# Optimization experiments

Hardware: AMD Instinct MI355X
Metric: run time of the kernel (lower is better)

Reference implementation:

```python
import jax, jax.numpy as jnp
import numpy as np

EPS = 1e-5
DILATIONS = (1, 2, 4)


def conv2d(x, w, b, pad, groups=1, dil=1):
    # x [B,C,H,W], w [O, C//groups, kh, kw]
    y = jax.lax.conv_general_dilated(
        x, w, window_strides=(1, 1),
        padding=[(pad[0], pad[0]), (pad[1], pad[1])],
        rhs_dilation=(dil, dil),
        dimension_numbers=('NCHW', 'OIHW', 'NCHW'),
        feature_group_count=groups)
    return y + b[None, :, None, None]


def bn(x, p):
    # inference BatchNorm2d; p rows = gamma, beta, mean, var
    g, b, m, v = p[0], p[1], p[2], p[3]
    scale = g * jax.lax.rsqrt(v + EPS)
    return x * scale[None, :, None, None] + (b - m * scale)[None, :, None, None]


def bilinear_sample(img, yy, xx):
    # img [C,H,W]; yy,xx [K,H,W] float sampling coords; zero outside -> [C,K,H,W]
    H, W = img.shape[1], img.shape[2]
    y0f = jnp.floor(yy); x0f = jnp.floor(xx)
    wy1 = yy - y0f; wy0 = 1.0 - wy1
    wx1 = xx - x0f; wx0 = 1.0 - wx1

    def gather(yi, xi):
        valid = (yi >= 0) & (yi < H) & (xi >= 0) & (xi < W)
        yc = jnp.clip(yi, 0, H - 1).astype(jnp.int32)
        xc = jnp.clip(xi, 0, W - 1).astype(jnp.int32)
        v = img[:, yc, xc]  # [C,K,H,W]
        return v * valid.astype(img.dtype)

    y1f = y0f + 1.0; x1f = x0f + 1.0
    return (gather(y0f, x0f) * (wy0 * wx0) + gather(y0f, x1f) * (wy0 * wx1)
            + gather(y1f, x0f) * (wy1 * wx0) + gather(y1f, x1f) * (wy1 * wx1))


def deform_depthwise(x, off, weight, dil):
    # torchvision DeformConv2d, groups=C, kernel 3x3, stride 1, pad=dil, no bias.
    # x [B,C,H,W], off [B,18,H,W] (per-kernel-point (dy,dx)), weight [C,3,3]
    B, C, H, W = x.shape
    off = off.reshape(B, 9, 2, H, W)
    hh = jnp.arange(H, dtype=x.dtype)[:, None]
    ww = jnp.arange(W, dtype=x.dtype)[None, :]
    k = jnp.arange(3, dtype=x.dtype) - 1.0
    ky = jnp.repeat(k, 3)  # [9] row offsets
    kx = jnp.tile(k, 3)    # [9] col offsets
    w9 = weight.reshape(C, 9)

    def per_batch(xb, offb):
        yy = offb[:, 0] + hh[None] + (ky * dil)[:, None, None]  # [9,H,W]
        xx = offb[:, 1] + ww[None] + (kx * dil)[:, None, None]
        s = bilinear_sample(xb, yy, xx)  # [C,9,H,W]
        return jnp.einsum('ckhw,ck->chw', s, w9)

    return jax.vmap(per_batch)(x, off)


def setup_inputs() -> dict:
    key = jax.random.key(0)
    ks = jax.random.split(key, 20)
    B, C, H, W = 2, 64, 192, 192
    r = jax.random.normal
    u = lambda k, s: jax.random.uniform(k, s, minval=0.5, maxval=1.5)
    return {
        'x': r(ks[0], (B, C, H, W)),
        'w_off1': r(ks[1], (C, 1, 1, 15)) * 0.1, 'b_off1': r(ks[2], (C,)) * 0.1,
        'bn_off1': u(ks[3], (4, C)),
        'w_off2': r(ks[4], (C, 1, 15, 1)) * 0.1, 'b_off2': r(ks[5], (C,)) * 0.1,
        'bn_off2': u(ks[6], (4, C)),
        'w_off3': r(ks[7], (C, 1, 3, 3)) * 0.1, 'b_off3': r(ks[8], (C,)) * 0.1,
        'bn_off3': u(ks[9], (4, C)),
        'w_bal_off': r(ks[10], (18, C, 1, 1)) * 0.1, 'b_bal_off': r(ks[11], (18,)) * 0.1,
        'bn_bal_off': u(ks[12], (4, 18)),
        'w_def': r(ks[13], (3, C, 3, 3)) * 0.1,
        'w_bal': r(ks[14], (C, C, 1, 1)) * 0.1, 'b_bal': r(ks[15], (C,)) * 0.1,
        'bn_bal': u(ks[16], (4, C)),
    }


def reference(x, w_off1, b_off1, bn_off1, w_off2, b_off2, bn_off2,
              w_off3, b_off3, bn_off3, w_bal_off, b_bal_off, bn_bal_off,
              w_def, w_bal, b_bal, bn_bal):
    C = x.shape[1]
    # DirectionOffsets: three depthwise conv+BN branches summed, then 1x1 conv+BN -> 18ch
    off_sum = (bn(conv2d(x, w_off1, b_off1, (0, 7), groups=C), bn_off1)
               + bn(conv2d(x, w_off2, b_off2, (7, 0), groups=C), bn_off2)
               + bn(conv2d(x, w_off3, b_off3, (1, 1), groups=C), bn_off3))
    offsets = bn(conv2d(off_sum, w_bal_off, b_bal_off, (0, 0)), bn_bal_off)  # [B,18,H,W]
    # sum of depthwise deformable conv branches (shared offsets, different dilation)
    deform_sum = sum(deform_depthwise(x, offsets, w_def[i], float(d))
                     for i, d in enumerate(DILATIONS))
    # final balance (1x1 conv + BN) gated by x
    return bn(conv2d(deform_sum, w_bal, b_bal, (0, 0)), bn_bal) * x
```

## Files before the change

### kernel.cpp

```cpp
#include <hip/hip_runtime.h>
#include <stdint.h>

constexpr int B = 2, C = 64, H = 192, W = 192;
constexpr int HW = H * W;
constexpr int P = B * H * W;
constexpr float EPS = 1e-5f;

__device__ __forceinline__ int swz(int bid, int nwg) {
  return (bid & 7) * (nwg >> 3) + (bid >> 3);
}

__global__ __launch_bounds__(256) void k_prepw(const float* __restrict__ w1,
    const float* __restrict__ w2, const float* __restrict__ w3,
    const float* __restrict__ wdef, float* __restrict__ w1t,
    float* __restrict__ w2t, float* __restrict__ w3t, float* __restrict__ wdeft) {
  int gid = blockIdx.x * 256 + threadIdx.x;
  const int stride = 8 * 256;
  for (int i = gid; i < 960; i += stride) {
    int c = i & 63, j = i >> 6;
    w1t[i] = w1[c * 15 + j];
    w2t[i] = w2[c * 15 + j];
  }
  for (int i = gid; i < 576; i += stride) {
    int c = i & 63, j = i >> 6;
    w3t[i] = w3[c * 9 + j];
  }
  for (int i = gid; i < 1728; i += stride) {
    int c = i & 63, jk = i >> 6;
    int di = jk / 9, k = jk % 9;
    wdeft[i] = wdef[di * (C * 9) + c * 9 + k];
  }
}

__global__ __launch_bounds__(256) void k_transpose(const float* __restrict__ x,
                                                   float* __restrict__ xt) {
  int blk = swz(blockIdx.x, B * H * (W / 64));
  int wt  = blk % (W / 64);
  int h   = (blk / (W / 64)) % H;
  int b   = blk / ((W / 64) * H);
  int w0  = wt * 64;
  __shared__ float tile[64][65];
  int tx = threadIdx.x & 63;
  int ty = threadIdx.x >> 6;
  #pragma unroll
  for (int c = ty; c < 64; c += 4)
    tile[c][tx] = x[((b * C + c) * H + h) * W + w0 + tx];
  __syncthreads();
  #pragma unroll
  for (int wi = ty; wi < 64; wi += 4)
    xt[((b * H + h) * W + w0 + wi) * 64 + tx] = tile[tx][wi];
}

__global__ __launch_bounds__(256) void k_offpipe(const float* __restrict__ xt,
    const float* __restrict__ w1t, const float* __restrict__ b1, const float* __restrict__ bn1,
    const float* __restrict__ w2t, const float* __restrict__ b2, const float* __restrict__ bn2,
    const float* __restrict__ w3t, const float* __restrict__ b3, const float* __restrict__ bn3,
    const float* __restrict__ wq, const float* __restrict__ bq, const float* __restrict__ bnq,
    float* __restrict__ offs) {
  __shared__ float os[16][68];
  __shared__ float wqs[18][66];
  __shared__ float qsc[18], qsh[18];

  int blk = swz(blockIdx.x, P / 16);
  int w0t = (blk % (W / 16)) * 16;
  int h   = (blk / (W / 16)) % H;
  int b   = blk / ((W / 16) * H);
  int wl  = threadIdx.x >> 6;
  int c   = threadIdx.x & 63;
  int w0  = w0t + wl * 4;
  const float* xb = xt + (size_t)b * HW * 64 + c;

  for (int i = threadIdx.x; i < 18 * 64; i += 256)
    wqs[i >> 6][i & 63] = wq[i];
  if (threadIdx.x < 18) {
    int o = threadIdx.x;
    float sc = bnq[o] / sqrtf(bnq[54 + o] + EPS);
    qsc[o] = sc;
    qsh[o] = fmaf(bq[o], sc, bnq[18 + o] - bnq[36 + o] * sc);
  }

  float s1[4] = {0.f, 0.f, 0.f, 0.f};
  float s2[4] = {0.f, 0.f, 0.f, 0.f};
  float s3[4] = {0.f, 0.f, 0.f, 0.f};
  {
    float xv[18];
    #pragma unroll
    for (int j = 0; j < 18; ++j) {
      int ww = w0 - 7 + j;
      xv[j] = (ww >= 0 && ww < W) ? xb[(h * W + ww) * 64] : 0.f;
    }
    #pragma unroll
    for (int j = 0; j < 15; ++j) {
      float wj = w1t[j * 64 + c];
      #pragma unroll
      for (int p = 0; p < 4; ++p) s1[p] = fmaf(xv[p + j], wj, s1[p]);
    }
  }
  #pragma unroll
  for (int j = 0; j < 15; ++j) {
    int hh = h - 7 + j;
    if (hh >= 0 && hh < H) {
      float wj = w2t[j * 64 + c];
      #pragma unroll
      for (int p = 0; p < 4; ++p)
        s2[p] = fmaf(xb[(hh * W + w0 + p) * 64], wj, s2[p]);
    }
  }
  #pragma unroll
  for (int dy = -1; dy <= 1; ++dy) {
    int hh = h + dy;
    if (hh >= 0 && hh < H) {
      float rv[6];
      #pragma unroll
      for (int j = 0; j < 6; ++j) {
        int ww = w0 - 1 + j;
        rv[j] = (ww >= 0 && ww < W) ? xb[(hh * W + ww) * 64] : 0.f;
      }
      #pragma unroll
      for (int dx = 0; dx < 3; ++dx) {
        float wj = w3t[((dy + 1) * 3 + dx) * 64 + c];
        #pragma unroll
        for (int p = 0; p < 4; ++p) s3[p] = fmaf(rv[p + dx], wj, s3[p]);
      }
    }
  }
  float sc1 = bn1[c] / sqrtf(bn1[192 + c] + EPS);
  float sh1 = bn1[64 + c] - bn1[128 + c] * sc1;
  float sc2 = bn2[c] / sqrtf(bn2[192 + c] + EPS);
  float sh2 = bn2[64 + c] - bn2[128 + c] * sc2;
  float sc3 = bn3[c] / sqrtf(bn3[192 + c] + EPS);
  float sh3 = bn3[64 + c] - bn3[128 + c] * sc3;
  float bb1 = b1[c], bb2 = b2[c], bb3 = b3[c];
  #pragma unroll
  for (int p = 0; p < 4; ++p)
    os[wl * 4 + p][c] =
        fmaf(s1[p] + bb1, sc1, sh1) + fmaf(s2[p] + bb2, sc2, sh2) +
        fmaf(s3[p] + bb3, sc3, sh3);
  __syncthreads();

  int p  = threadIdx.x & 15;
  int og = threadIdx.x >> 4;
  float dreg[64];
  #pragma unroll
  for (int q = 0; q < 16; ++q) {
    float4 v = *(float4*)&os[p][q * 4];
    dreg[4 * q + 0] = v.x; dreg[4 * q + 1] = v.y;
    dreg[4 * q + 2] = v.z; dreg[4 * q + 3] = v.w;
  }
  size_t pix = (size_t)((b * H + h) * W + w0t + p);
  #pragma unroll
  for (int pass = 0; pass < 2; ++pass) {
    int o = (pass == 0) ? og : 16 + og;
    if (pass == 1 && og >= 2) break;
    float a0 = 0.f, a1 = 0.f, a2 = 0.f, a3 = 0.f;
    #pragma unroll
    for (int q = 0; q < 16; ++q) {
      float4 ww = *(float4*)&wqs[o][q * 4];
      a0 = fmaf(dreg[4 * q + 0], ww.x, a0);
      a1 = fmaf(dreg[4 * q + 1], ww.y, a1);
      a2 = fmaf(dreg[4 * q + 2], ww.z, a2);
      a3 = fmaf(dreg[4 * q + 3], ww.w, a3);
    }
    float s = (a0 + a1) + (a2 + a3);
    offs[pix * 18 + o] = fmaf(s, qsc[o], qsh[o]);
  }
}

__global__ __launch_bounds__(256) void k_deform(const float* __restrict__ xt,
                                                const float* __restrict__ offs,
                                                const float* __restrict__ wdeft,
                                                float* __restrict__ dsum) {
  __shared__ uint32_t lpre[4][27 * 8 + 4];
  int wl   = threadIdx.x >> 6;
  int lane = threadIdx.x & 63;
  int pix  = swz(blockIdx.x, P / 4) * 4 + wl;

  if (lane < 27) {
    int di = lane / 9, k = lane % 9;
    int d  = 1 << di;
    int w = pix % W, h = (pix / W) % H;
    float offy = offs[(size_t)pix * 18 + 2 * k];
    float offx = offs[(size_t)pix * 18 + 2 * k + 1];
    int ky = k / 3 - 1, kx = k % 3 - 1;
    float yy = (offy + (float)h) + (float)(ky * d);
    float xx = (offx + (float)w) + (float)(kx * d);
    float y0f = floorf(yy), x0f = floorf(xx);
    float wy1 = yy - y0f, wx1 = xx - x0f;
    float wy0 = 1.f - wy1, wx0 = 1.f - wx1;
    int y0 = (int)fmaxf(fminf(y0f, 1.0e4f), -1.0e4f);
    int x0 = (int)fmaxf(fminf(x0f, 1.0e4f), -1.0e4f);
    int y1 = y0 + 1, x1 = x0 + 1;
    float my0 = (y0 >= 0 && y0 < H) ? 1.f : 0.f;
    float my1 = (y1 >= 0 && y1 < H) ? 1.f : 0.f;
    float mx0 = (x0 >= 0 && x0 < W) ? 1.f : 0.f;
    float mx1 = (x1 >= 0 && x1 < W) ? 1.f : 0.f;
    int y0c = min(max(y0, 0), H - 1), y1c = min(max(y1, 0), H - 1);
    int x0c = min(max(x0, 0), W - 1), x1c = min(max(x1, 0), W - 1);
    int r0 = y0c * W, r1 = y1c * W;
    float wy0m = wy0 * my0, wy1m = wy1 * my1;
    float wx0m = wx0 * mx0, wx1m = wx1 * mx1;
    uint32_t* q = &lpre[wl][lane * 8];
    q[0] = (uint32_t)(r0 + x0c) << 8;
    q[1] = (uint32_t)(r0 + x1c) << 8;
    q[2] = (uint32_t)(r1 + x0c) << 8;
    q[3] = (uint32_t)(r1 + x1c) << 8;
    q[4] = __float_as_uint(wy0m * wx0m);
    q[5] = __float_as_uint(wy0m * wx1m);
    q[6] = __float_as_uint(wy1m * wx0m);
    q[7] = __float_as_uint(wy1m * wx1m);
  }
  __syncthreads();

  int c = lane;
  int b = pix / HW;
  const char* xb0 = (const char*)(xt + (size_t)b * HW * 64);

  float wd[27];
  #pragma unroll
  for (int i = 0; i < 27; ++i) wd[i] = wdeft[i * 64 + c];

  float acc = 0.f;
  #pragma unroll
  for (int t = 0; t < 27; ++t) {
    uint4 ov = *(const uint4*)&lpre[wl][t * 8];
    uint4 wv = *(const uint4*)&lpre[wl][t * 8 + 4];
    int s00 = __builtin_amdgcn_readfirstlane((int)ov.x);
    int s01 = __builtin_amdgcn_readfirstlane((int)ov.y);
    int s10 = __builtin_amdgcn_readfirstlane((int)ov.z);
    int s11 = __builtin_amdgcn_readfirstlane((int)ov.w);
    const float* p00 = (const float*)(xb0 + s00);
    const float* p01 = (const float*)(xb0 + s01);
    const float* p10 = (const float*)(xb0 + s10);
    const float* p11 = (const float*)(xb0 + s11);
    float v00 = p00[c], v01 = p01[c], v10 = p10[c], v11 = p11[c];
    float bil = fmaf(v11, __uint_as_float(wv.w),
                 fmaf(v10, __uint_as_float(wv.z),
                  fmaf(v01, __uint_as_float(wv.y),
                       v00 * __uint_as_float(wv.x))));
    acc = fmaf(wd[t], bil, acc);
  }
  dsum[(size_t)pix * 64 + c] = acc;
}

__global__ __launch_bounds__(256) void k_final(const float* __restrict__ ds,
    const float* __restrict__ x, const float* __restrict__ wb,
    const float* __restrict__ bb, const float* __restrict__ bnb,
    float* __restrict__ out) {
  int blk = swz(blockIdx.x, P / 64);
  int w0 = (blk % (W / 64)) * 64;
  int h  = (blk / (W / 64)) % H;
  int b  = blk / ((W / 64) * H);
  __shared__ float dtile[64][68];
  __shared__ float scs[64], shb[64];
  int tx = threadIdx.x & 63;
  int ty = threadIdx.x >> 6;
  int pixbase = (b * H + h) * W + w0;

  {
    int pr  = threadIdx.x >> 4;
    int ic4 = (threadIdx.x & 15) * 4;
    #pragma unroll
    for (int pass = 0; pass < 4; ++pass) {
      int pix = pass * 16 + pr;
      float4 v = *(const float4*)&ds[(size_t)(pixbase + pix) * 64 + ic4];
      *(float4*)&dtile[pix][ic4] = v;
    }
  }
  if (threadIdx.x < 64) {
    float g = bnb[threadIdx.x], vv = bnb[192 + threadIdx.x];
    float sc = g / sqrtf(vv + EPS);
    scs[threadIdx.x] = sc;
    shb[threadIdx.x] = fmaf(bb[threadIdx.x], sc,
                            bnb[64 + threadIdx.x] - bnb[128 + threadIdx.x] * sc);
  }
  __syncthreads();

  float dreg[64];
  #pragma unroll
  for (int q = 0; q < 16; ++q) {
    float4 v = *(float4*)&dtile[tx][q * 4];
    dreg[4 * q + 0] = v.x; dreg[4 * q + 1] = v.y;
    dreg[4 * q + 2] = v.z; dreg[4 * q + 3] = v.w;
  }

  int ocb = __builtin_amdgcn_readfirstlane(ty);
  #pragma unroll
  for (int j = 0; j < 16; ++j) {
    int oc = ocb + 4 * j;
    const float* wr = wb + oc * 64;
    float a0 = 0.f, a1 = 0.f, a2 = 0.f, a3 = 0.f;
    #pragma unroll
    for (int q = 0; q < 16; ++q) {
      a0 = fmaf(dreg[4 * q + 0], wr[4 * q + 0], a0);
      a1 = fmaf(dreg[4 * q + 1], wr[4 * q + 1], a1);
      a2 = fmaf(dreg[4 * q + 2], wr[4 * q + 2], a2);
      a3 = fmaf(dreg[4 * q + 3], wr[4 * q + 3], a3);
    }
    float s = (a0 + a1) + (a2 + a3);
    float val = fmaf(s, scs[oc], shb[oc]);
    int xi = ((b * C + oc) * H + h) * W + w0 + tx;
    out[xi] = val * x[xi];
  }
}

extern "C" void kernel_launch(void* const* d_in, const int* in_sizes, int n_in,
                              void* d_out, int out_size, void* d_ws, size_t ws_size,
                              hipStream_t stream) {
  const float* x     = (const float*)d_in[0];
  const float* w1    = (const float*)d_in[1];
  const float* b1    = (const float*)d_in[2];
  const float* bn1   = (const float*)d_in[3];
  const float* w2    = (const float*)d_in[4];
  const float* b2    = (const float*)d_in[5];
  const float* bn2   = (const float*)d_in[6];
  const float* w3    = (const float*)d_in[7];
  const float* b3    = (const float*)d_in[8];
  const float* bn3   = (const float*)d_in[9];
  const float* wbo   = (const float*)d_in[10];
  const float* bbo   = (const float*)d_in[11];
  const float* bnbo  = (const float*)d_in[12];
  const float* wdef  = (const float*)d_in[13];
  const float* wbal  = (const float*)d_in[14];
  const float* bbal  = (const float*)d_in[15];
  const float* bnbal = (const float*)d_in[16];
  float* out = (float*)d_out;

  float* xt    = (float*)d_ws;
  float* dsum  = xt + (size_t)P * 64;
  float* offs  = dsum + (size_t)P * 64;
  float* wts   = offs + (size_t)P * 18;
  float* w1t   = wts;
  float* w2t   = wts + 960;
  float* w3t   = wts + 1920;
  float* wdeft = wts + 2496;

  k_prepw<<<8, 256, 0, stream>>>(w1, w2, w3, wdef, w1t, w2t, w3t, wdeft);
  k_transpose<<<B * H * (W / 64), 256, 0, stream>>>(x, xt);
  k_offpipe<<<P / 16, 256, 0, stream>>>(xt, w1t, b1, bn1, w2t, b2, bn2,
                                        w3t, b3, bn3, wbo, bbo, bnbo, offs);
  k_deform<<<P / 4, 256, 0, stream>>>(xt, offs, wdeft, dsum);
  k_final<<<P / 64, 256, 0, stream>>>(dsum, x, wbal, bbal, bnbal, out);
}
```

Before: 244.7 us.

## Keep deform sample coords in registers, dedupe center taps, fold weight prep

The per-pixel bilinear sample coordinates and weights are now computed in registers by every lane and broadcast with readlane, replacing the LDS staging buffer and the block barrier. The center tap (k=4) is the same for all three dilations, so it is sampled once and reused for the three weights, dropping two of the 27 gathers per pixel. The separate weight-transpose kernel is merged into the transpose kernel to save one launch. All lanes now repeat the coordinate math, which adds some redundant ALU work.

```diff
diff --git a/kernel.cpp b/kernel.cpp
--- a/kernel.cpp
+++ b/kernel.cpp
@@ -10,30 +10,30 @@
   return (bid & 7) * (nwg >> 3) + (bid >> 3);
 }
 
-__global__ __launch_bounds__(256) void k_prepw(const float* __restrict__ w1,
-    const float* __restrict__ w2, const float* __restrict__ w3,
-    const float* __restrict__ wdef, float* __restrict__ w1t,
-    float* __restrict__ w2t, float* __restrict__ w3t, float* __restrict__ wdeft) {
-  int gid = blockIdx.x * 256 + threadIdx.x;
-  const int stride = 8 * 256;
-  for (int i = gid; i < 960; i += stride) {
-    int c = i & 63, j = i >> 6;
-    w1t[i] = w1[c * 15 + j];
-    w2t[i] = w2[c * 15 + j];
-  }
-  for (int i = gid; i < 576; i += stride) {
-    int c = i & 63, j = i >> 6;
-    w3t[i] = w3[c * 9 + j];
-  }
-  for (int i = gid; i < 1728; i += stride) {
-    int c = i & 63, jk = i >> 6;
-    int di = jk / 9, k = jk % 9;
-    wdeft[i] = wdef[di * (C * 9) + c * 9 + k];
-  }
-}
-
 __global__ __launch_bounds__(256) void k_transpose(const float* __restrict__ x,
-                                                   float* __restrict__ xt) {
+    float* __restrict__ xt,
+    const float* __restrict__ w1, const float* __restrict__ w2,
+    const float* __restrict__ w3, const float* __restrict__ wdef,
+    float* __restrict__ w1t, float* __restrict__ w2t,
+    float* __restrict__ w3t, float* __restrict__ wdeft) {
+  if (blockIdx.x < 8) {
+    int gid = blockIdx.x * 256 + threadIdx.x;
+    const int stride = 8 * 256;
+    for (int i = gid; i < 960; i += stride) {
+      int c = i & 63, j = i >> 6;
+      w1t[i] = w1[c * 15 + j];
+      w2t[i] = w2[c * 15 + j];
+    }
+    for (int i = gid; i < 576; i += stride) {
+      int c = i & 63, j = i >> 6;
+      w3t[i] = w3[c * 9 + j];
+    }
+    for (int i = gid; i < 1728; i += stride) {
+      int c = i & 63, jk = i >> 6;
+      int di = jk / 9, k = jk % 9;
+      wdeft[i] = wdef[di * (C * 9) + c * 9 + k];
+    }
+  }
   int blk = swz(blockIdx.x, B * H * (W / 64));
   int wt  = blk % (W / 64);
   int h   = (blk / (W / 64)) % H;
@@ -170,17 +170,21 @@
                                                 const float* __restrict__ offs,
                                                 const float* __restrict__ wdeft,
                                                 float* __restrict__ dsum) {
-  __shared__ uint32_t lpre[4][27 * 8 + 4];
   int wl   = threadIdx.x >> 6;
   int lane = threadIdx.x & 63;
   int pix  = swz(blockIdx.x, P / 4) * 4 + wl;
 
-  if (lane < 27) {
-    int di = lane / 9, k = lane % 9;
+  int li = lane;
+  if (li >= 54) li -= 54;
+  if (li >= 27) li -= 27;
+  int di = li / 9, k = li % 9;
+  uint32_t o00, o01, o10, o11, bw00, bw01, bw10, bw11;
+  {
     int d  = 1 << di;
     int w = pix % W, h = (pix / W) % H;
-    float offy = offs[(size_t)pix * 18 + 2 * k];
-    float offx = offs[(size_t)pix * 18 + 2 * k + 1];
+    const float* op = offs + (size_t)pix * 18;
+    float offy = op[2 * k];
+    float offx = op[2 * k + 1];
     int ky = k / 3 - 1, kx = k % 3 - 1;
     float yy = (offy + (float)h) + (float)(ky * d);
     float xx = (offx + (float)w) + (float)(kx * d);
@@ -199,17 +203,15 @@
     int r0 = y0c * W, r1 = y1c * W;
     float wy0m = wy0 * my0, wy1m = wy1 * my1;
     float wx0m = wx0 * mx0, wx1m = wx1 * mx1;
-    uint32_t* q = &lpre[wl][lane * 8];
-    q[0] = (uint32_t)(r0 + x0c) << 8;
-    q[1] = (uint32_t)(r0 + x1c) << 8;
-    q[2] = (uint32_t)(r1 + x0c) << 8;
-    q[3] = (uint32_t)(r1 + x1c) << 8;
-    q[4] = __float_as_uint(wy0m * wx0m);
-    q[5] = __float_as_uint(wy0m * wx1m);
-    q[6] = __float_as_uint(wy1m * wx0m);
-    q[7] = __float_as_uint(wy1m * wx1m);
-  }
-  __syncthreads();
+    o00 = (uint32_t)(r0 + x0c) << 8;
+    o01 = (uint32_t)(r0 + x1c) << 8;
+    o10 = (uint32_t)(r1 + x0c) << 8;
+    o11 = (uint32_t)(r1 + x1c) << 8;
+    bw00 = __float_as_uint(wy0m * wx0m);
+    bw01 = __float_as_uint(wy0m * wx1m);
+    bw10 = __float_as_uint(wy1m * wx0m);
+    bw11 = __float_as_uint(wy1m * wx1m);
+  }
 
   int c = lane;
   int b = pix / HW;
@@ -222,22 +224,28 @@
   float acc = 0.f;
   #pragma unroll
   for (int t = 0; t < 27; ++t) {
-    uint4 ov = *(const uint4*)&lpre[wl][t * 8];
-    uint4 wv = *(const uint4*)&lpre[wl][t * 8 + 4];
-    int s00 = __builtin_amdgcn_readfirstlane((int)ov.x);
-    int s01 = __builtin_amdgcn_readfirstlane((int)ov.y);
-    int s10 = __builtin_amdgcn_readfirstlane((int)ov.z);
-    int s11 = __builtin_amdgcn_readfirstlane((int)ov.w);
+    if (t == 13 || t == 22) continue;
+    int s00 = __builtin_amdgcn_readlane((int)o00, t);
+    int s01 = __builtin_amdgcn_readlane((int)o01, t);
+    int s10 = __builtin_amdgcn_readlane((int)o10, t);
+    int s11 = __builtin_amdgcn_readlane((int)o11, t);
+    float w00 = __uint_as_float(__builtin_amdgcn_readlane((int)bw00, t));
+    float w01 = __uint_as_float(__builtin_amdgcn_readlane((int)bw01, t));
+    float w10 = __uint_as_float(__builtin_amdgcn_readlane((int)bw10, t));
+    float w11 = __uint_as_float(__builtin_amdgcn_readlane((int)bw11, t));
     const float* p00 = (const float*)(xb0 + s00);
     const float* p01 = (const float*)(xb0 + s01);
     const float* p10 = (const float*)(xb0 + s10);
     const float* p11 = (const float*)(xb0 + s11);
     float v00 = p00[c], v01 = p01[c], v10 = p10[c], v11 = p11[c];
-    float bil = fmaf(v11, __uint_as_float(wv.w),
-                 fmaf(v10, __uint_as_float(wv.z),
-                  fmaf(v01, __uint_as_float(wv.y),
-                       v00 * __uint_as_float(wv.x))));
-    acc = fmaf(wd[t], bil, acc);
+    float bil = fmaf(v11, w11, fmaf(v10, w10, fmaf(v01, w01, v00 * w00)));
+    if (t == 4) {
+      acc = fmaf(wd[4], bil, acc);
+      acc = fmaf(wd[13], bil, acc);
+      acc = fmaf(wd[22], bil, acc);
+    } else {
+      acc = fmaf(wd[t], bil, acc);
+    }
   }
   dsum[(size_t)pix * 64 + c] = acc;
 }
@@ -334,8 +342,8 @@
   float* w3t   = wts + 1920;
   float* wdeft = wts + 2496;
 
-  k_prepw<<<8, 256, 0, stream>>>(w1, w2, w3, wdef, w1t, w2t, w3t, wdeft);
-  k_transpose<<<B * H * (W / 64), 256, 0, stream>>>(x, xt);
+  k_transpose<<<B * H * (W / 64), 256, 0, stream>>>(x, xt, w1, w2, w3, wdef,
+                                                    w1t, w2t, w3t, wdeft);
   k_offpipe<<<P / 16, 256, 0, stream>>>(xt, w1t, b1, bn1, w2t, b2, bn2,
                                         w3t, b3, bn3, wbo, bbo, bnbo, offs);
   k_deform<<<P / 4, 256, 0, stream>>>(xt, offs, wdeft, dsum);
```

After: 251.8 us. 1.03x slower.

## Vectorize deform gathers across corners, merge center taps, fold weight prep into transpose

Applied to the files above, without the earlier changes.

The deformable conv kernel now splits each wavefront into four 16-lane groups, one per bilinear corner. Each lane loads a float4 of channels, and a small LDS reduction then sums the four corner partials. The three center taps (k=4 across dilations) sample the same location because they share offsets, so their weights are pre-summed into one extra row and two of the three taps are skipped. The weight-transposing kernel is merged into the transpose kernel to save a launch. In exchange it adds an extra __syncthreads and LDS traffic per block.

```diff
diff --git a/kernel.cpp b/kernel.cpp
--- a/kernel.cpp
+++ b/kernel.cpp
@@ -10,30 +10,33 @@
   return (bid & 7) * (nwg >> 3) + (bid >> 3);
 }
 
-__global__ __launch_bounds__(256) void k_prepw(const float* __restrict__ w1,
-    const float* __restrict__ w2, const float* __restrict__ w3,
-    const float* __restrict__ wdef, float* __restrict__ w1t,
-    float* __restrict__ w2t, float* __restrict__ w3t, float* __restrict__ wdeft) {
-  int gid = blockIdx.x * 256 + threadIdx.x;
-  const int stride = 8 * 256;
-  for (int i = gid; i < 960; i += stride) {
-    int c = i & 63, j = i >> 6;
-    w1t[i] = w1[c * 15 + j];
-    w2t[i] = w2[c * 15 + j];
-  }
-  for (int i = gid; i < 576; i += stride) {
-    int c = i & 63, j = i >> 6;
-    w3t[i] = w3[c * 9 + j];
-  }
-  for (int i = gid; i < 1728; i += stride) {
-    int c = i & 63, jk = i >> 6;
-    int di = jk / 9, k = jk % 9;
-    wdeft[i] = wdef[di * (C * 9) + c * 9 + k];
-  }
-}
-
 __global__ __launch_bounds__(256) void k_transpose(const float* __restrict__ x,
-                                                   float* __restrict__ xt) {
+    float* __restrict__ xt,
+    const float* __restrict__ w1, const float* __restrict__ w2,
+    const float* __restrict__ w3, const float* __restrict__ wdef,
+    float* __restrict__ w1t, float* __restrict__ w2t,
+    float* __restrict__ w3t, float* __restrict__ wdeft) {
+  if (blockIdx.x < 8) {
+    int gid = blockIdx.x * 256 + threadIdx.x;
+    const int stride = 8 * 256;
+    for (int i = gid; i < 960; i += stride) {
+      int c = i & 63, j = i >> 6;
+      w1t[i] = w1[c * 15 + j];
+      w2t[i] = w2[c * 15 + j];
+    }
+    for (int i = gid; i < 576; i += stride) {
+      int c = i & 63, j = i >> 6;
+      w3t[i] = w3[c * 9 + j];
+    }
+    for (int i = gid; i < 1728; i += stride) {
+      int c = i & 63, jk = i >> 6;
+      int di = jk / 9, k = jk % 9;
+      wdeft[i] = wdef[di * (C * 9) + c * 9 + k];
+    }
+    for (int i = gid; i < 64; i += stride)
+      wdeft[27 * 64 + i] =
+          wdef[i * 9 + 4] + wdef[576 + i * 9 + 4] + wdef[1152 + i * 9 + 4];
+  }
   int blk = swz(blockIdx.x, B * H * (W / 64));
   int wt  = blk % (W / 64);
   int h   = (blk / (W / 64)) % H;
@@ -170,7 +173,8 @@
                                                 const float* __restrict__ offs,
                                                 const float* __restrict__ wdeft,
                                                 float* __restrict__ dsum) {
-  __shared__ uint32_t lpre[4][27 * 8 + 4];
+  __shared__ uint32_t lpre[4][27 * 8];
+  __shared__ float racc[4][4 * 64];
   int wl   = threadIdx.x >> 6;
   int lane = threadIdx.x & 63;
   int pix  = swz(blockIdx.x, P / 4) * 4 + wl;
@@ -179,8 +183,9 @@
     int di = lane / 9, k = lane % 9;
     int d  = 1 << di;
     int w = pix % W, h = (pix / W) % H;
-    float offy = offs[(size_t)pix * 18 + 2 * k];
-    float offx = offs[(size_t)pix * 18 + 2 * k + 1];
+    const float* op = offs + (size_t)pix * 18;
+    float offy = op[2 * k];
+    float offx = op[2 * k + 1];
     int ky = k / 3 - 1, kx = k % 3 - 1;
     float yy = (offy + (float)h) + (float)(ky * d);
     float xx = (offx + (float)w) + (float)(kx * d);
@@ -211,35 +216,31 @@
   }
   __syncthreads();
 
-  int c = lane;
+  int g = lane >> 4;
+  int l = lane & 15;
   int b = pix / HW;
-  const char* xb0 = (const char*)(xt + (size_t)b * HW * 64);
-
-  float wd[27];
-  #pragma unroll
-  for (int i = 0; i < 27; ++i) wd[i] = wdeft[i * 64 + c];
-
-  float acc = 0.f;
+  const char* xb0 = (const char*)(xt + (size_t)b * HW * 64) + l * 16;
+
+  float4 acc = {0.f, 0.f, 0.f, 0.f};
   #pragma unroll
   for (int t = 0; t < 27; ++t) {
-    uint4 ov = *(const uint4*)&lpre[wl][t * 8];
-    uint4 wv = *(const uint4*)&lpre[wl][t * 8 + 4];
-    int s00 = __builtin_amdgcn_readfirstlane((int)ov.x);
-    int s01 = __builtin_amdgcn_readfirstlane((int)ov.y);
-    int s10 = __builtin_amdgcn_readfirstlane((int)ov.z);
-    int s11 = __builtin_amdgcn_readfirstlane((int)ov.w);
-    const float* p00 = (const float*)(xb0 + s00);
-    const float* p01 = (const float*)(xb0 + s01);
-    const float* p10 = (const float*)(xb0 + s10);
-    const float* p11 = (const float*)(xb0 + s11);
-    float v00 = p00[c], v01 = p01[c], v10 = p10[c], v11 = p11[c];
-    float bil = fmaf(v11, __uint_as_float(wv.w),
-                 fmaf(v10, __uint_as_float(wv.z),
-                  fmaf(v01, __uint_as_float(wv.y),
-                       v00 * __uint_as_float(wv.x))));
-    acc = fmaf(wd[t], bil, acc);
-  }
-  dsum[(size_t)pix * 64 + c] = acc;
+    if (t == 13 || t == 22) continue;
+    uint32_t off = lpre[wl][t * 8 + g];
+    float wgt = __uint_as_float(lpre[wl][t * 8 + 4 + g]);
+    float4 v = *(const float4*)(xb0 + off);
+    const int wrow = (t == 4) ? 27 : t;
+    float4 wd = *(const float4*)&wdeft[wrow * 64 + 4 * l];
+    acc.x = fmaf(v.x * wgt, wd.x, acc.x);
+    acc.y = fmaf(v.y * wgt, wd.y, acc.y);
+    acc.z = fmaf(v.z * wgt, wd.z, acc.z);
+    acc.w = fmaf(v.w * wgt, wd.w, acc.w);
+  }
+
+  *(float4*)&racc[wl][g * 64 + 4 * l] = acc;
+  __syncthreads();
+  float s = racc[wl][lane] + racc[wl][64 + lane] +
+            racc[wl][128 + lane] + racc[wl][192 + lane];
+  dsum[(size_t)pix * 64 + lane] = s;
 }
 
 __global__ __launch_bounds__(256) void k_final(const float* __restrict__ ds,
@@ -334,8 +335,8 @@
   float* w3t   = wts + 1920;
   float* wdeft = wts + 2496;
 
-  k_prepw<<<8, 256, 0, stream>>>(w1, w2, w3, wdef, w1t, w2t, w3t, wdeft);
-  k_transpose<<<B * H * (W / 64), 256, 0, stream>>>(x, xt);
+  k_transpose<<<B * H * (W / 64), 256, 0, stream>>>(x, xt, w1, w2, w3, wdef,
+                                                    w1t, w2t, w3t, wdeft);
   k_offpipe<<<P / 16, 256, 0, stream>>>(xt, w1t, b1, bn1, w2t, b2, bn2,
                                         w3t, b3, bn3, wbo, bbo, bnbo, offs);
   k_deform<<<P / 4, 256, 0, stream>>>(xt, offs, wdeft, dsum);
```

New measurement: 271.4 us. +10.9%, slower.
